# Optimization experiments

Hardware: AMD Instinct MI355X
Metric: run time of the kernel (lower is better)

The kernel has to match this reference:

```python
import jax, jax.numpy as jnp
import numpy as np

B, S0, S1 = 4, 768, 256
T = S0 + S1
D0, D1 = 2048, 1024
N, K, H = 8, 1, 256  # num_heads, num_kv_heads, head_dim
G = N // K
BIG_NEG = -2.3819763e38


def _apply_rope(x, positions, max_wavelength=10000):
    # x: [B, L, Hn, Hd]; positions: [B, L] float32
    half = x.shape[-1] // 2
    freq_exponents = (2.0 / x.shape[-1]) * jnp.arange(half, dtype=jnp.float32)
    timescale = max_wavelength ** freq_exponents
    radians = positions[..., None] / timescale[None, None, :]   # [B, L, half]
    radians = radians[..., None, :]                             # [B, L, 1, half]
    sin, cos = jnp.sin(radians), jnp.cos(radians)
    x1, x2 = jnp.split(x, 2, axis=-1)
    res = jnp.concatenate([x1 * cos - x2 * sin, x2 * cos + x1 * sin], axis=-1)
    return res.astype(x.dtype)


def setup_inputs() -> dict:
    key = jax.random.key(0)
    ks = jax.random.split(key, 8)
    x0 = jax.random.normal(ks[0], (B, S0, D0), dtype=jnp.float32)
    x1 = jax.random.normal(ks[1], (B, S1, D1), dtype=jnp.float32)
    positions = jnp.broadcast_to(jnp.arange(T, dtype=jnp.float32), (B, T))
    # causal mask [B, 1, T, T]
    attn_mask = jnp.broadcast_to(jnp.tril(jnp.ones((T, T), dtype=bool)), (B, 1, T, T))
    # lecun_normal-style init: std = 1/sqrt(fan_in=width)
    q0_w = jax.random.normal(ks[2], (N, D0, H), dtype=jnp.float32) * (D0 ** -0.5)
    kv0_w = jax.random.normal(ks[3], (2, K, D0, H), dtype=jnp.float32) * (D0 ** -0.5)
    q1_w = jax.random.normal(ks[4], (N, D1, H), dtype=jnp.float32) * (D1 ** -0.5)
    kv1_w = jax.random.normal(ks[5], (2, K, D1, H), dtype=jnp.float32) * (D1 ** -0.5)
    o0_w = jax.random.normal(ks[6], (N, H, D0), dtype=jnp.float32) * ((N * H) ** -0.5)
    o1_w = jax.random.normal(ks[7], (N, H, D1), dtype=jnp.float32) * ((N * H) ** -0.5)
    return {"x0": x0, "x1": x1, "positions": positions, "attn_mask": attn_mask,
            "q0_w": q0_w, "kv0_w": kv0_w, "q1_w": q1_w, "kv1_w": kv1_w,
            "o0_w": o0_w, "o1_w": o1_w}


def reference(x0, x1, positions, attn_mask, q0_w, kv0_w, q1_w, kv1_w, o0_w, o1_w):
    dtype = x0.dtype
    # per-stream GQA projections (num_kv_heads != num_heads path)
    q_a = jnp.einsum('BTD,NDH->BTNH', x0, q0_w)
    kv_a = jnp.einsum('BSD,CKDH->CBSKH', x0, kv0_w)
    q_b = jnp.einsum('BTD,NDH->BTNH', x1, q1_w)
    kv_b = jnp.einsum('BSD,CKDH->CBSKH', x1, kv1_w)
    # concat streams along sequence
    q = jnp.concatenate([q_a, q_b], axis=1)                 # [B, T, N, H]
    k = jnp.concatenate([kv_a[0], kv_b[0]], axis=1)         # [B, T, K, H]
    v = jnp.concatenate([kv_a[1], kv_b[1]], axis=1)         # [B, T, K, H]
    # inline RoPE + query scaling
    q = _apply_rope(q, positions) * (H ** -0.5)
    k = _apply_rope(k, positions)
    # GQA grouping: N = K * G
    qg = q.reshape(q.shape[0], q.shape[1], K, G, H)          # [B, T, K, G, H]
    logits = jnp.einsum('BTKGH,BSKH->BKGTS', qg, k,
                        preferred_element_type=jnp.float32)  # fp32 scores
    masked = jnp.where(attn_mask[:, :, None, :, :], logits, BIG_NEG)
    probs = jax.nn.softmax(masked, axis=-1).astype(dtype)
    encoded = jnp.einsum('BKGTS,BSKH->BTKGH', probs, v)
    encoded = encoded.reshape(encoded.shape[0], encoded.shape[1], N, H)  # [B, T, N, H]
    out0 = jnp.einsum('BTNH,NHD->BTD', encoded[:, :S0], o0_w)
    out1 = jnp.einsum('BTNH,NHD->BTD', encoded[:, S0:], o1_w)
    return (out0, out1)
```

## Files before the change

kernel.cpp:

```cpp
#include <hip/hip_runtime.h>

typedef unsigned short u16;
typedef __attribute__((ext_vector_type(8))) short bf16x8;
typedef __attribute__((ext_vector_type(4))) float f32x4;

#define CB   4
#define CS0  768
#define CS1  256
#define CT   1024
#define CD0  2048
#define CD1  1024
#define CN   8
#define CH   256
#define IDENT (1 << 30)
#define BIGBASE 0x7fffffff

__device__ __forceinline__ float bf2f(u16 u) {
    union { unsigned int i; float f; } v;
    v.i = ((unsigned int)u) << 16;
    return v.f;
}
__device__ __forceinline__ u16 f2bf(float f) {
    union { float f; unsigned int i; } v;
    v.f = f;
    unsigned int r = 0x7fffu + ((v.i >> 16) & 1u);
    return (u16)((v.i + r) >> 16);
}

__device__ __forceinline__ void gl_lds16(const u16* g, u16* lds_base) {
    __builtin_amdgcn_global_load_lds(
        (const __attribute__((address_space(1))) void*)g,
        (__attribute__((address_space(3))) void*)lds_base,
        16, 0, 0);
}

struct PSeg { const float* in; u16* out; int R, C, base, lgx, lgy, mode; };
struct PSeg8 { PSeg t[8]; };

__global__ __launch_bounds__(256) void prep_multi(PSeg8 segs)
{
    __shared__ float tl[32][33];
    int bid = blockIdx.x;
    PSeg g = segs.t[0];
    #pragma unroll
    for (int i = 1; i < 8; i++)
        if (bid >= segs.t[i].base) g = segs.t[i];
    int r = bid - g.base;
    if (g.mode == 0) {
        int i = r * 256 + threadIdx.x;
        float4 v = ((const float4*)g.in)[i];
        ushort4 o;
        o.x = f2bf(v.x); o.y = f2bf(v.y); o.z = f2bf(v.z); o.w = f2bf(v.w);
        ((ushort4*)g.out)[i] = o;
    } else {
        int bx = r & ((1 << g.lgx) - 1);
        int by = (r >> g.lgx) & ((1 << g.lgy) - 1);
        int bz = r >> (g.lgx + g.lgy);
        const float* in = g.in + (size_t)bz * g.R * g.C;
        u16* out = g.out + (size_t)bz * g.R * g.C;
        int c0 = bx * 32, r0 = by * 32;
        int tx = threadIdx.x & 31, ty = threadIdx.x >> 5;
        #pragma unroll
        for (int i = 0; i < 32; i += 8)
            tl[ty + i][tx] = in[(size_t)(r0 + ty + i) * g.C + c0 + tx];
        __syncthreads();
        #pragma unroll
        for (int i = 0; i < 32; i += 8)
            out[(size_t)(c0 + ty + i) * g.R + r0 + tx] = f2bf(tl[tx][ty + i]);
    }
}

struct GSeg {
    const u16* A; const u16* BT; void* C;
    int K, Cstride, base, lgnx;
    int Sa, Ta, ta, Sc, Tc, tc, obf, pad;
};
struct GSeg4 { GSeg s[4]; };

__global__ __launch_bounds__(256, 3) void gemm128_multi(GSeg4 segs)
{
    __shared__ __align__(16) u16 lds[3 * 8192];

    int bid = blockIdx.x;
    GSeg g = segs.s[0];
    if (bid >= segs.s[1].base) g = segs.s[1];
    if (bid >= segs.s[2].base) g = segs.s[2];
    if (bid >= segs.s[3].base) g = segs.s[3];

    int tid  = threadIdx.x;
    int r    = bid - g.base;
    int n0   = (r & ((1 << g.lgnx) - 1)) * 128;
    int m0   = (r >> g.lgnx) * 128;
    int wave = tid >> 6, lane = tid & 63;

    int srow  = tid >> 2;
    int skoff = ((tid & 3) ^ ((srow >> 1) & 3)) * 8;
    int am1 = m0 + srow, am2 = m0 + 64 + srow;
    const u16* aptr1 = g.A + (size_t)((am1 / g.Sa) * g.Ta + g.ta + am1 % g.Sa) * g.K + skoff;
    const u16* aptr2 = g.A + (size_t)((am2 / g.Sa) * g.Ta + g.ta + am2 % g.Sa) * g.K + skoff;
    const u16* bptr1 = g.BT + (size_t)(n0 + srow) * g.K + skoff;
    const u16* bptr2 = g.BT + (size_t)(n0 + 64 + srow) * g.K + skoff;

    int mw = (wave >> 1) * 64, nw = (wave & 1) * 64;
    int l15 = lane & 15;
    int q4  = lane >> 4;
    int sw  = (q4 ^ ((l15 >> 1) & 3)) * 8;

#define STAGE(bufi, tt) do { int kk = (tt) * 32; \
        u16* base = lds + (bufi) * 8192 + wave * 512; \
        gl_lds16(aptr1 + kk, base); \
        gl_lds16(aptr2 + kk, base + 2048); \
        gl_lds16(bptr1 + kk, base + 4096); \
        gl_lds16(bptr2 + kk, base + 6144); } while (0)

    f32x4 acc[4][4] = {};
    int nkt = g.K >> 5;

    STAGE(0, 0);
    STAGE(1, 1);

    int cur = 0, nxt = 2;
    for (int t = 0; t < nkt; ++t) {
        if (t + 1 < nkt) asm volatile("s_waitcnt vmcnt(4)" ::: "memory");
        else             asm volatile("s_waitcnt vmcnt(0)" ::: "memory");
        __builtin_amdgcn_sched_barrier(0);
        __builtin_amdgcn_s_barrier();
        asm volatile("" ::: "memory");
        if (t + 2 < nkt) STAGE(nxt, t + 2);

        const u16* At = lds + cur * 8192;
        const u16* Bt = At + 4096;
        bf16x8 af[4], bfr[4];
        #pragma unroll
        for (int i = 0; i < 4; i++)
            af[i] = *(const bf16x8*)&At[(mw + i * 16 + l15) * 32 + sw];
        #pragma unroll
        for (int i = 0; i < 4; i++)
            bfr[i] = *(const bf16x8*)&Bt[(nw + i * 16 + l15) * 32 + sw];
        asm volatile("s_waitcnt lgkmcnt(0)" ::: "memory");
        __builtin_amdgcn_sched_barrier(0);
        __builtin_amdgcn_s_setprio(1);
        #pragma unroll
        for (int mi = 0; mi < 4; mi++)
            #pragma unroll
            for (int ni = 0; ni < 4; ni++)
                acc[mi][ni] = __builtin_amdgcn_mfma_f32_16x16x32_bf16(
                    af[mi], bfr[ni], acc[mi][ni], 0, 0, 0);
        __builtin_amdgcn_s_setprio(0);
        cur = (cur == 2) ? 0 : cur + 1;
        nxt = (nxt == 2) ? 0 : nxt + 1;
    }
#undef STAGE

    #pragma unroll
    for (int mi = 0; mi < 4; mi++) {
        #pragma unroll
        for (int rr = 0; rr < 4; rr++) {
            int mm = m0 + mw + mi * 16 + q4 * 4 + rr;
            int grow = (mm / g.Sc) * g.Tc + g.tc + mm % g.Sc;
            if (g.obf) {
                u16* crow = (u16*)g.C + (size_t)grow * g.Cstride + n0 + nw + l15;
                #pragma unroll
                for (int ni = 0; ni < 4; ni++)
                    crow[ni * 16] = f2bf(acc[mi][ni][rr]);
            } else {
                float* crow = (float*)g.C + (size_t)grow * g.Cstride + n0 + nw + l15;
                #pragma unroll
                for (int ni = 0; ni < 4; ni++)
                    crow[ni * 16] = acc[mi][ni][rr];
            }
        }
    }
}

__global__ __launch_bounds__(256) void rope_vt_kernel(
    const u16* __restrict__ qsrc, const u16* __restrict__ kvsrc,
    const float* __restrict__ positions,
    u16* __restrict__ qb, u16* __restrict__ kb, u16* __restrict__ vto)
{
    int bid = blockIdx.x;
    if (bid < 18432) {
        int idx = bid * 256 + threadIdx.x;
        const int QP = CB * CT * CN * 128;
        if (idx < QP) {
            int h  = idx & 127;
            int n  = (idx >> 7) & 7;
            int bt = idx >> 10;
            const u16* base = qsrc + (size_t)bt * 2048 + n * 256;
            float pos = positions[bt];
            float ts  = powf(10000.0f, (float)h * (1.0f / 128.0f));
            float rr  = pos / ts;
            float sn = sinf(rr), cs = cosf(rr);
            float x1 = bf2f(base[h]), x2 = bf2f(base[h + 128]);
            u16* ob = qb + (size_t)bt * 2048 + n * 256;
            ob[h]       = f2bf((x1 * cs - x2 * sn) * 0.0625f);
            ob[h + 128] = f2bf((x2 * cs + x1 * sn) * 0.0625f);
        } else {
            int j  = idx - QP;
            int h  = j & 127;
            int bt = j >> 7;
            const u16* base = kvsrc + (size_t)bt * 512;
            float pos = positions[bt];
            float ts  = powf(10000.0f, (float)h * (1.0f / 128.0f));
            float rr  = pos / ts;
            float sn = sinf(rr), cs = cosf(rr);
            float x1 = bf2f(base[h]), x2 = bf2f(base[h + 128]);
            int b = bt >> 10, t = bt & 1023;
            int h2 = h + 128;
            kb[((size_t)(b * 8 + (h  >> 5)) * 1024 + t) * 32 + (h  & 31)] = f2bf(x1 * cs - x2 * sn);
            kb[((size_t)(b * 8 + (h2 >> 5)) * 1024 + t) * 32 + (h2 & 31)] = f2bf(x2 * cs + x1 * sn);
        }
    } else {
        int vb = bid - 18432;
        int h  = threadIdx.x;
        int sc = vb & 31;
        int b  = vb >> 5;
        const u16* src = kvsrc + ((size_t)(b * 1024 + sc * 32) * 512 + 256 + h);
        u16* dst = vto + ((size_t)(b * 32 + sc) * 256 + h) * 32;
        u16 buf[32];
        #pragma unroll
        for (int ss = 0; ss < 32; ss++)
            buf[ss] = src[(size_t)ss * 512];
        #pragma unroll
        for (int i = 0; i < 8; i++)
            ((ushort4*)dst)[i] = ((ushort4*)buf)[i];
    }
}

__global__ __launch_bounds__(128) void flash_attn(
    const u16* __restrict__ qb, const u16* __restrict__ kb,
    const u16* __restrict__ vt, u16* __restrict__ encoded)
{
    __shared__ __align__(16) u16 Ks[8192];
    __shared__ __align__(16) u16 Vs[8192];
    __shared__ __align__(16) u16 Pw[2][640];

    int tid  = threadIdx.x;
    int wave = tid >> 6, lane = tid & 63;
    int q4 = lane >> 4, l15 = lane & 15;
    int swz = (q4 ^ ((l15 >> 1) & 3)) * 8;

    int bid  = blockIdx.x;
    int half = bid >> 9;
    int r    = bid & 511;
    int b    = (half << 1) | (r >> 8);
    int qi   = r & 255;
    if (half) qi = 255 - qi;
    int t0 = qi * 4;

    bf16x8 af[8];
    {
        int m = wave * 16 + l15;
        int head = m >> 2, tl = m & 3;
        const u16* qrow = qb + ((size_t)(b * CT + t0 + tl) * 2048 + head * 256 + q4 * 8);
        #pragma unroll
        for (int kc = 0; kc < 8; kc++)
            af[kc] = *(const bf16x8*)(qrow + kc * 32);
    }

    f32x4 O[16] = {};
    float lrun[4] = {0.f, 0.f, 0.f, 0.f};

    int send = t0 + 4;
    int nt   = (send + 31) >> 5;

    for (int t = 0; t < nt; ++t) {
        int s0 = t * 32;
        if (t) __syncthreads();
        #pragma unroll
        for (int is = 0; is < 8; ++is) {
            int ubase = is * 128 + wave * 64;
            int u = ubase + lane;
            int gK = u & 3, sK = (u >> 2) & 31, hc = u >> 7;
            int ug = gK ^ ((sK >> 1) & 3);
            const u16* gp = kb + ((size_t)((b * 8 + hc) * 1024 + s0 + sK) * 32 + ug * 8);
            gl_lds16(gp, Ks + (size_t)ubase * 8);
        }
        #pragma unroll
        for (int is = 0; is < 8; ++is) {
            int ubase = is * 128 + wave * 64;
            int u = ubase + lane;
            int gV = u & 3, hv = u >> 2;
            int vg = gV ^ ((hv >> 1) & 3);
            const u16* gp = vt + ((size_t)(b * 32 + (s0 >> 5)) * 8192 + (size_t)hv * 32 + vg * 8);
            gl_lds16(gp, Vs + (size_t)ubase * 8);
        }
        __syncthreads();

        f32x4 P[2];
        #pragma unroll
        for (int ni = 0; ni < 2; ni++) {
            f32x4 c = {};
            #pragma unroll
            for (int kc = 0; kc < 8; kc++) {
                bf16x8 bfr = *(const bf16x8*)&Ks[kc * 1024 + (ni * 16 + l15) * 32 + swz];
                c = __builtin_amdgcn_mfma_f32_16x16x32_bf16(af[kc], bfr, c, 0, 0, 0);
            }
            P[ni] = c;
        }

        if (t == nt - 1) {
            #pragma unroll
            for (int ni = 0; ni < 2; ni++)
                #pragma unroll
                for (int rr = 0; rr < 4; rr++) {
                    int trow = t0 + rr;
                    int scol = s0 + ni * 16 + l15;
                    if (scol > trow) P[ni][rr] = -3.0e38f;
                }
        }

        #pragma unroll
        for (int ni = 0; ni < 2; ni++)
            #pragma unroll
            for (int rr = 0; rr < 4; rr++) {
                float e = __expf(P[ni][rr]);
                P[ni][rr] = e;
                Pw[wave][(q4 * 4 + rr) * 40 + ni * 16 + l15] = f2bf(e);
            }
        #pragma unroll
        for (int rr = 0; rr < 4; rr++) {
            float s = P[0][rr] + P[1][rr];
            s += __shfl_xor(s, 1);
            s += __shfl_xor(s, 2);
            s += __shfl_xor(s, 4);
            s += __shfl_xor(s, 8);
            lrun[rr] += s;
        }

        bf16x8 pa = *(const bf16x8*)&Pw[wave][l15 * 40 + q4 * 8];
        #pragma unroll
        for (int nc = 0; nc < 16; nc++) {
            bf16x8 b0 = *(const bf16x8*)&Vs[(nc * 16 + l15) * 32 + swz];
            O[nc] = __builtin_amdgcn_mfma_f32_16x16x32_bf16(pa, b0, O[nc], 0, 0, 0);
        }
    }

    #pragma unroll
    for (int rr = 0; rr < 4; rr++) {
        int mm = wave * 16 + q4 * 4 + rr;
        int hd = mm >> 2, tl = mm & 3;
        u16* erow = encoded + ((size_t)(b * CT + t0 + tl) * 2048 + hd * 256 + l15);
        float inv = 1.0f / lrun[rr];
        #pragma unroll
        for (int nc = 0; nc < 16; nc++)
            erow[nc * 16] = f2bf(O[nc][rr] * inv);
    }
}

extern "C" void kernel_launch(void* const* d_in, const int* in_sizes, int n_in,
                              void* d_out, int out_size, void* d_ws, size_t ws_size,
                              hipStream_t stream)
{
    const float* x0        = (const float*)d_in[0];
    const float* x1        = (const float*)d_in[1];
    const float* positions = (const float*)d_in[2];
    const float* q0_w  = (const float*)d_in[4];
    const float* kv0_w = (const float*)d_in[5];
    const float* q1_w  = (const float*)d_in[6];
    const float* kv1_w = (const float*)d_in[7];
    const float* o0_w  = (const float*)d_in[8];
    const float* o1_w  = (const float*)d_in[9];
    float* out = (float*)d_out;

    char* W = (char*)d_ws;
    u16* qbuf16  = (u16*)(W);
    u16* kvbuf16 = (u16*)(W + 16777216);
    u16* WTo0  = (u16*)(W + 20971520);
    u16* WTo1  = (u16*)(W + 29360128);
    u16* x0b   = (u16*)(W + 33554432);
    u16* x1b   = (u16*)(W + 46137344);
    u16* WTq0  = (u16*)(W + 48234496);
    u16* WTkv0 = (u16*)(W + 56623104);
    u16* WTq1  = (u16*)(W + 58720256);
    u16* WTkv1 = (u16*)(W + 62914560);
    u16* qb  = x0b;
    u16* kb  = WTkv0;
    u16* vtb = WTq1;
    u16* encoded = qbuf16;

    PSeg8 ps8;
    ps8.t[0] = { x0,    x0b,      0,    0,     0, 0, 0, 0 };
    ps8.t[1] = { x1,    x1b,      0,    0,  6144, 0, 0, 0 };
    ps8.t[2] = { q0_w,  WTq0,  2048,  256,  7168, 3, 6, 1 };
    ps8.t[3] = { kv0_w, WTkv0, 2048,  256, 11264, 3, 6, 1 };
    ps8.t[4] = { q1_w,  WTq1,  1024,  256, 12288, 3, 5, 1 };
    ps8.t[5] = { kv1_w, WTkv1, 1024,  256, 14336, 3, 5, 1 };
    ps8.t[6] = { o0_w,  WTo0,  2048, 2048, 14848, 6, 6, 1 };
    ps8.t[7] = { o1_w,  WTo1,  2048, 1024, 18944, 5, 6, 1 };
    prep_multi<<<dim3(20992), dim3(256), 0, stream>>>(ps8);

    GSeg4 ps;
    ps.s[0] = { x0b, WTq0,  qbuf16,  2048, 2048,   0, 4, IDENT, 0, 0, CS0, CT, 0,   1, 0 };
    ps.s[1] = { x0b, WTkv0, kvbuf16, 2048,  512, 384, 2, IDENT, 0, 0, CS0, CT, 0,   1, 0 };
    ps.s[2] = { x1b, WTq1,  qbuf16,  1024, 2048, 480, 4, IDENT, 0, 0, CS1, CT, CS0, 1, 0 };
    ps.s[3] = { x1b, WTkv1, kvbuf16, 1024,  512, 608, 2, IDENT, 0, 0, CS1, CT, CS0, 1, 0 };
    gemm128_multi<<<dim3(640), dim3(256), 0, stream>>>(ps);

    rope_vt_kernel<<<dim3(18560), dim3(256), 0, stream>>>(
        qbuf16, kvbuf16, positions, qb, kb, vtb);

    flash_attn<<<dim3(1024), dim3(128), 0, stream>>>(qb, kb, vtb, encoded);

    GSeg4 os;
    os.s[0] = { encoded, WTo0, out, 2048, 2048,   0, 4, CS0, CT, 0,   IDENT, 0, 0, 0, 0 };
    os.s[1] = { encoded, WTo1, out + (size_t)CB * CS0 * CD0,
                2048, 1024, 384, 3, CS1, CT, CS0, IDENT, 0, 0, 0, 0 };
    os.s[2] = { nullptr, nullptr, nullptr, 128, 0, BIGBASE, 0, 1, 0, 0, 1, 0, 0, 0, 0 };
    os.s[3] = { nullptr, nullptr, nullptr, 128, 0, BIGBASE, 0, 1, 0, 0, 1, 0, 0, 0, 0 };
    gemm128_multi<<<dim3(448), dim3(256), 0, stream>>>(os);
}
```

Before: 314.4 us.

## Use single-wave flash attention blocks reading K/V directly from global memory

The attention kernel goes from two waves per block sharing K/V tiles staged in shared memory to one wave per block. That wave covers all 32 query rows (two 16-row MFMA tiles) and loads K and V fragments straight from global memory into registers. Each K/V fragment now feeds two MFMAs, and the block-wide barriers and LDS staging disappear. The cost is more registers (doubled O accumulators), dependence on the L1/L2 cache for K/V reuse, and lost latency hiding from the async global-to-LDS copies. The block order also changes to interleave batches with longest-first query chunks.

```diff
diff --git a/kernel.cpp b/kernel.cpp
--- a/kernel.cpp
+++ b/kernel.cpp
@@ -227,124 +227,101 @@
     }
 }
 
-__global__ __launch_bounds__(128) void flash_attn(
+__global__ __launch_bounds__(64, 2) void flash_attn(
     const u16* __restrict__ qb, const u16* __restrict__ kb,
     const u16* __restrict__ vt, u16* __restrict__ encoded)
 {
-    __shared__ __align__(16) u16 Ks[8192];
-    __shared__ __align__(16) u16 Vs[8192];
-    __shared__ __align__(16) u16 Pw[2][640];
-
-    int tid  = threadIdx.x;
-    int wave = tid >> 6, lane = tid & 63;
+    __shared__ __align__(16) u16 Pw[32 * 40];
+
+    int lane = threadIdx.x & 63;
     int q4 = lane >> 4, l15 = lane & 15;
-    int swz = (q4 ^ ((l15 >> 1) & 3)) * 8;
-
-    int bid  = blockIdx.x;
-    int half = bid >> 9;
-    int r    = bid & 511;
-    int b    = (half << 1) | (r >> 8);
-    int qi   = r & 255;
-    if (half) qi = 255 - qi;
-    int t0 = qi * 4;
-
-    bf16x8 af[8];
-    {
-        int m = wave * 16 + l15;
-        int head = m >> 2, tl = m & 3;
-        const u16* qrow = qb + ((size_t)(b * CT + t0 + tl) * 2048 + head * 256 + q4 * 8);
+
+    int bid = blockIdx.x;
+    int b   = bid & 3;
+    int qc  = 255 - (bid >> 2);
+    int t0  = qc * 4;
+    int nt  = (t0 + 4 + 31) >> 5;
+
+    bf16x8 af[2][8];
+    #pragma unroll
+    for (int mi = 0; mi < 2; mi++) {
+        int m = mi * 16 + l15;
+        const u16* qrow = qb + ((size_t)(b * CT + t0 + (m & 3)) * 2048 + (m >> 2) * 256 + q4 * 8);
         #pragma unroll
         for (int kc = 0; kc < 8; kc++)
-            af[kc] = *(const bf16x8*)(qrow + kc * 32);
-    }
-
-    f32x4 O[16] = {};
-    float lrun[4] = {0.f, 0.f, 0.f, 0.f};
-
-    int send = t0 + 4;
-    int nt   = (send + 31) >> 5;
+            af[mi][kc] = *(const bf16x8*)(qrow + kc * 32);
+    }
+
+    f32x4 O[2][16] = {};
+    float sacc[2][4] = {};
 
     for (int t = 0; t < nt; ++t) {
         int s0 = t * 32;
-        if (t) __syncthreads();
-        #pragma unroll
-        for (int is = 0; is < 8; ++is) {
-            int ubase = is * 128 + wave * 64;
-            int u = ubase + lane;
-            int gK = u & 3, sK = (u >> 2) & 31, hc = u >> 7;
-            int ug = gK ^ ((sK >> 1) & 3);
-            const u16* gp = kb + ((size_t)((b * 8 + hc) * 1024 + s0 + sK) * 32 + ug * 8);
-            gl_lds16(gp, Ks + (size_t)ubase * 8);
-        }
-        #pragma unroll
-        for (int is = 0; is < 8; ++is) {
-            int ubase = is * 128 + wave * 64;
-            int u = ubase + lane;
-            int gV = u & 3, hv = u >> 2;
-            int vg = gV ^ ((hv >> 1) & 3);
-            const u16* gp = vt + ((size_t)(b * 32 + (s0 >> 5)) * 8192 + (size_t)hv * 32 + vg * 8);
-            gl_lds16(gp, Vs + (size_t)ubase * 8);
-        }
-        __syncthreads();
-
-        f32x4 P[2];
-        #pragma unroll
-        for (int ni = 0; ni < 2; ni++) {
-            f32x4 c = {};
-            #pragma unroll
-            for (int kc = 0; kc < 8; kc++) {
-                bf16x8 bfr = *(const bf16x8*)&Ks[kc * 1024 + (ni * 16 + l15) * 32 + swz];
-                c = __builtin_amdgcn_mfma_f32_16x16x32_bf16(af[kc], bfr, c, 0, 0, 0);
+
+        f32x4 P[2][2] = {};
+        #pragma unroll
+        for (int kc = 0; kc < 8; kc++) {
+            #pragma unroll
+            for (int ni = 0; ni < 2; ni++) {
+                bf16x8 bk = *(const bf16x8*)(kb +
+                    ((size_t)((b * 8 + kc) * 1024 + s0 + ni * 16 + l15)) * 32 + q4 * 8);
+                P[0][ni] = __builtin_amdgcn_mfma_f32_16x16x32_bf16(af[0][kc], bk, P[0][ni], 0, 0, 0);
+                P[1][ni] = __builtin_amdgcn_mfma_f32_16x16x32_bf16(af[1][kc], bk, P[1][ni], 0, 0, 0);
             }
-            P[ni] = c;
         }
 
         if (t == nt - 1) {
+            #pragma unroll
+            for (int mi = 0; mi < 2; mi++)
+                #pragma unroll
+                for (int ni = 0; ni < 2; ni++)
+                    #pragma unroll
+                    for (int rr = 0; rr < 4; rr++) {
+                        int scol = s0 + ni * 16 + l15;
+                        if (scol > t0 + rr) P[mi][ni][rr] = -3.0e38f;
+                    }
+        }
+
+        #pragma unroll
+        for (int mi = 0; mi < 2; mi++)
             #pragma unroll
             for (int ni = 0; ni < 2; ni++)
                 #pragma unroll
                 for (int rr = 0; rr < 4; rr++) {
-                    int trow = t0 + rr;
-                    int scol = s0 + ni * 16 + l15;
-                    if (scol > trow) P[ni][rr] = -3.0e38f;
+                    float e = __expf(P[mi][ni][rr]);
+                    sacc[mi][rr] += e;
+                    Pw[(mi * 16 + q4 * 4 + rr) * 40 + ni * 16 + l15] = f2bf(e);
                 }
-        }
-
-        #pragma unroll
-        for (int ni = 0; ni < 2; ni++)
-            #pragma unroll
-            for (int rr = 0; rr < 4; rr++) {
-                float e = __expf(P[ni][rr]);
-                P[ni][rr] = e;
-                Pw[wave][(q4 * 4 + rr) * 40 + ni * 16 + l15] = f2bf(e);
-            }
+
+        bf16x8 pa0 = *(const bf16x8*)&Pw[l15 * 40 + q4 * 8];
+        bf16x8 pa1 = *(const bf16x8*)&Pw[(16 + l15) * 40 + q4 * 8];
+        int sc = s0 >> 5;
+        #pragma unroll
+        for (int nc = 0; nc < 16; nc++) {
+            bf16x8 vv = *(const bf16x8*)(vt +
+                ((size_t)((b * 32 + sc) * 256 + nc * 16 + l15)) * 32 + q4 * 8);
+            O[0][nc] = __builtin_amdgcn_mfma_f32_16x16x32_bf16(pa0, vv, O[0][nc], 0, 0, 0);
+            O[1][nc] = __builtin_amdgcn_mfma_f32_16x16x32_bf16(pa1, vv, O[1][nc], 0, 0, 0);
+        }
+    }
+
+    #pragma unroll
+    for (int mi = 0; mi < 2; mi++) {
         #pragma unroll
         for (int rr = 0; rr < 4; rr++) {
-            float s = P[0][rr] + P[1][rr];
+            float s = sacc[mi][rr];
             s += __shfl_xor(s, 1);
             s += __shfl_xor(s, 2);
             s += __shfl_xor(s, 4);
             s += __shfl_xor(s, 8);
-            lrun[rr] += s;
-        }
-
-        bf16x8 pa = *(const bf16x8*)&Pw[wave][l15 * 40 + q4 * 8];
-        #pragma unroll
-        for (int nc = 0; nc < 16; nc++) {
-            bf16x8 b0 = *(const bf16x8*)&Vs[(nc * 16 + l15) * 32 + swz];
-            O[nc] = __builtin_amdgcn_mfma_f32_16x16x32_bf16(pa, b0, O[nc], 0, 0, 0);
-        }
-    }
-
-    #pragma unroll
-    for (int rr = 0; rr < 4; rr++) {
-        int mm = wave * 16 + q4 * 4 + rr;
-        int hd = mm >> 2, tl = mm & 3;
-        u16* erow = encoded + ((size_t)(b * CT + t0 + tl) * 2048 + hd * 256 + l15);
-        float inv = 1.0f / lrun[rr];
-        #pragma unroll
-        for (int nc = 0; nc < 16; nc++)
-            erow[nc * 16] = f2bf(O[nc][rr] * inv);
+            float inv = 1.0f / s;
+            int row = mi * 16 + q4 * 4 + rr;
+            int hd  = row >> 2;
+            u16* erow = encoded + ((size_t)(b * CT + t0 + rr) * 2048 + hd * 256 + l15);
+            #pragma unroll
+            for (int nc = 0; nc < 16; nc++)
+                erow[nc * 16] = f2bf(O[mi][nc][rr] * inv);
+        }
     }
 }
 
@@ -400,7 +377,7 @@
     rope_vt_kernel<<<dim3(18560), dim3(256), 0, stream>>>(
         qbuf16, kvbuf16, positions, qb, kb, vtb);
 
-    flash_attn<<<dim3(1024), dim3(128), 0, stream>>>(qb, kb, vtb, encoded);
+    flash_attn<<<dim3(1024), dim3(64), 0, stream>>>(qb, kb, vtb, encoded);
 
     GSeg4 os;
     os.s[0] = { encoded, WTo0, out, 2048, 2048,   0, 4, CS0, CT, 0,   IDENT, 0, 0, 0, 0 };
```

New measurement: 397.1 us. 26.3% more time.
